# Kernel tuning notes

Hardware: AMD Instinct MI355X
Metric: run time of the kernel (lower is better)

The kernel has to match this reference:

```python
import jax, jax.numpy as jnp
import numpy as np

B, N, EMB, H, DH = 1, 196, 256, 8, 32
HID = 4 * EMB
EPS = 1e-5
SCALE = 16.0  # emb_size ** 0.5 (torch code scales by emb_size, not head_dim)


def _ln(x, w, b):
    m = jnp.mean(x, axis=-1, keepdims=True)
    v = jnp.mean((x - m) ** 2, axis=-1, keepdims=True)
    return (x - m) * jax.lax.rsqrt(v + EPS) * w + b


def _qkv(x, W, bias):
    # rearrange 'b n (h d qkv) -> qkv b h n d'
    t = (x @ W + bias).reshape(B, N, H, DH, 3)
    t = jnp.transpose(t, (4, 0, 2, 1, 3))
    return t[0], t[1], t[2]


def _attn(q, k, v, Wp, bp):
    att = jax.nn.softmax(jnp.einsum('bhqd,bhkd->bhqk', q, k) / SCALE, axis=-1)
    o = jnp.einsum('bhqk,bhkd->bhqd', att, v)
    o = jnp.transpose(o, (0, 2, 1, 3)).reshape(B, N, EMB)  # b n (h d)
    return o @ Wp + bp


def _ff(x, W1, b1, W2, b2):
    return jax.nn.gelu(x @ W1 + b1, approximate=False) @ W2 + b2


def _recon(x):
    x = x.reshape(B, 14, 14, 16, 16)
    x = jnp.transpose(x, (0, 3, 4, 1, 2))
    return x.reshape(B, 1, 224, 224)


def setup_inputs() -> dict:
    key = jax.random.key(0)
    ks = jax.random.split(key, 16)
    rn = lambda k, shape: jax.random.normal(k, shape, jnp.float32) * 0.02
    d = {
        'vis_emb': jax.random.normal(ks[0], (B, N, EMB), jnp.float32),
        'ir_emb': jax.random.normal(ks[1], (B, N, EMB), jnp.float32),
        'ln1v_w': jnp.ones((EMB,), jnp.float32), 'ln1v_b': jnp.zeros((EMB,), jnp.float32),
        'ln1i_w': jnp.ones((EMB,), jnp.float32), 'ln1i_b': jnp.zeros((EMB,), jnp.float32),
        'ln2v_w': jnp.ones((EMB,), jnp.float32), 'ln2v_b': jnp.zeros((EMB,), jnp.float32),
        'ln2i_w': jnp.ones((EMB,), jnp.float32), 'ln2i_b': jnp.zeros((EMB,), jnp.float32),
        'Wqkv_v': rn(ks[2], (EMB, 3 * EMB)), 'bqkv_v': jnp.zeros((3 * EMB,), jnp.float32),
        'Wqkv_i': rn(ks[3], (EMB, 3 * EMB)), 'bqkv_i': jnp.zeros((3 * EMB,), jnp.float32),
        'Wp_v': rn(ks[4], (EMB, EMB)), 'bp_v': jnp.zeros((EMB,), jnp.float32),
        'Wp_i': rn(ks[5], (EMB, EMB)), 'bp_i': jnp.zeros((EMB,), jnp.float32),
        'W1v': rn(ks[6], (EMB, HID)), 'b1v': jnp.zeros((HID,), jnp.float32),
        'W2v': rn(ks[7], (HID, EMB)), 'b2v': jnp.zeros((EMB,), jnp.float32),
        'W1i': rn(ks[8], (EMB, HID)), 'b1i': jnp.zeros((HID,), jnp.float32),
        'W2i': rn(ks[9], (HID, EMB)), 'b2i': jnp.zeros((EMB,), jnp.float32),
    }
    return d


def reference(vis_emb, ir_emb, ln1v_w, ln1v_b, ln1i_w, ln1i_b, ln2v_w, ln2v_b,
              ln2i_w, ln2i_b, Wqkv_v, bqkv_v, Wqkv_i, bqkv_i, Wp_v, bp_v,
              Wp_i, bp_i, W1v, b1v, W2v, b2v, W1i, b1i, W2i, b2i):
    nv = _ln(vis_emb, ln1v_w, ln1v_b)
    ni = _ln(ir_emb, ln1i_w, ln1i_b)
    qv, kv_, vv = _qkv(vis_emb, Wqkv_v, bqkv_v)
    qi, ki, vi = _qkv(ir_emb, Wqkv_i, bqkv_i)
    cross_v2i = _attn(qv, ki, vi, Wp_v, bp_v)   # vis queries attend ir k/v
    cross_i2v = _attn(qi, kv_, vv, Wp_i, bp_i)  # ir queries attend vis k/v
    rv = nv + cross_v2i
    ri = ni + cross_i2v
    lv = _ln(rv, ln2v_w, ln2v_b)
    li = _ln(ri, ln2i_w, ln2i_b)
    ov = _ff(lv, W1v, b1v, W2v, b2v) + lv
    oi = _ff(li, W1i, b1i, W2i, b2i) + li
    return jnp.concatenate([_recon(oi), _recon(ov)], axis=1)  # (1,2,224,224)
```

## Files before the change

### kernel.cpp

```cpp
#include <hip/hip_runtime.h>
#include <math.h>

#define NT   196
#define EMB  256
#define NH   8
#define DH   32
#define HID  1024
#define EPSV 1e-5f

#define GEMM_PANEL(Wptr, ldw, xsT, pp, cq, ks, KITER)                          \
    {                                                                          \
        const float* Wb = (Wptr);                                              \
        float4 a0 = {0,0,0,0}, a1 = a0, a2 = a0, a3 = a0;                      \
        _Pragma("unroll 8")                                                    \
        for (int kk = (ks) * (KITER); kk < (ks) * (KITER) + (KITER); kk++) {   \
            float4 w4 = *(const float4*)&Wb[kk * (ldw)];                       \
            float4 xr = *(const float4*)&(xsT)[kk * 4];                        \
            a0.x = fmaf(xr.x, w4.x, a0.x); a0.y = fmaf(xr.x, w4.y, a0.y);      \
            a0.z = fmaf(xr.x, w4.z, a0.z); a0.w = fmaf(xr.x, w4.w, a0.w);      \
            a1.x = fmaf(xr.y, w4.x, a1.x); a1.y = fmaf(xr.y, w4.y, a1.y);      \
            a1.z = fmaf(xr.y, w4.z, a1.z); a1.w = fmaf(xr.y, w4.w, a1.w);      \
            a2.x = fmaf(xr.z, w4.x, a2.x); a2.y = fmaf(xr.z, w4.y, a2.y);      \
            a2.z = fmaf(xr.z, w4.z, a2.z); a2.w = fmaf(xr.z, w4.w, a2.w);      \
            a3.x = fmaf(xr.w, w4.x, a3.x); a3.y = fmaf(xr.w, w4.y, a3.y);      \
            a3.z = fmaf(xr.w, w4.z, a3.z); a3.w = fmaf(xr.w, w4.w, a3.w);      \
        }                                                                      \
        *(float4*)&(pp)[((ks) * 4 + 0) * 256 + (cq) * 4] = a0;                 \
        *(float4*)&(pp)[((ks) * 4 + 1) * 256 + (cq) * 4] = a1;                 \
        *(float4*)&(pp)[((ks) * 4 + 2) * 256 + (cq) * 4] = a2;                 \
        *(float4*)&(pp)[((ks) * 4 + 3) * 256 + (cq) * 4] = a3;                 \
    }

__global__ __launch_bounds__(256) void k1_qkv(
    const float* __restrict__ vis, const float* __restrict__ ir,
    const float* __restrict__ Wqkv_v, const float* __restrict__ bqkv_v,
    const float* __restrict__ Wqkv_i, const float* __restrict__ bqkv_i,
    float* __restrict__ Q, float* __restrict__ Kq, float* __restrict__ Vq)
{
    const int b = blockIdx.x;
    const int s = b / 147;
    const int rem = b % 147;
    const int n0 = (rem / 3) * 4;
    const int cg = rem % 3;
    const int t = threadIdx.x;

    const float* x    = (s == 0) ? vis    : ir;
    const float* W    = (s == 0) ? Wqkv_v : Wqkv_i;
    const float* bias = (s == 0) ? bqkv_v : bqkv_i;

    __shared__ float xsT[EMB * 4];
    __shared__ float pp[4 * 4 * 256];

    {
        int r = t >> 6, c4 = (t & 63) * 4;
        float4 xv = *(const float4*)&x[(n0 + r) * EMB + c4];
        xsT[(c4 + 0) * 4 + r] = xv.x;
        xsT[(c4 + 1) * 4 + r] = xv.y;
        xsT[(c4 + 2) * 4 + r] = xv.z;
        xsT[(c4 + 3) * 4 + r] = xv.w;
    }
    __syncthreads();

    const int cq = t & 63, ks = t >> 6;
    GEMM_PANEL(W + cg * 256 + cq * 4, 768, xsT, pp, cq, ks, 64);
    __syncthreads();

    const int col = cg * 256 + t;
    const int h = col / 96, rr = col % 96, d = rr / 3, q = rr % 3;
    float* dst = (q == 0) ? Q : (q == 1 ? Kq : Vq);
    const float bval = bias[col];
    #pragma unroll
    for (int r = 0; r < 4; r++) {
        float v = pp[(0 * 4 + r) * 256 + t] + pp[(1 * 4 + r) * 256 + t]
                + pp[(2 * 4 + r) * 256 + t] + pp[(3 * 4 + r) * 256 + t] + bval;
        dst[((s * NH + h) * NT + n0 + r) * DH + d] = v;
    }
}

__global__ __launch_bounds__(256) void k2_attn(
    const float* __restrict__ Q, const float* __restrict__ Kq,
    const float* __restrict__ Vq, float* __restrict__ AO)
{
    const int b  = blockIdx.x;
    const int s  = b / 112;
    const int rm = b % 112;
    const int h  = rm / 14;
    const int rt = rm % 14;
    const int t    = threadIdx.x;
    const int wv   = t >> 6;
    const int lane = t & 63;

    __shared__ float kl[NT * 33];
    __shared__ float vl[NT * 33];
    __shared__ float pb[4][NT];

    const float4* Ks4 = (const float4*)(Kq + ((1 - s) * NH + h) * NT * DH);
    const float4* Vs4 = (const float4*)(Vq + ((1 - s) * NH + h) * NT * DH);
    for (int idx = t; idx < NT * 8; idx += 256) {
        int j = idx >> 3, d4 = (idx & 7) * 4;
        float4 kv = Ks4[idx];
        kl[j * 33 + d4 + 0] = kv.x; kl[j * 33 + d4 + 1] = kv.y;
        kl[j * 33 + d4 + 2] = kv.z; kl[j * 33 + d4 + 3] = kv.w;
        float4 vv = Vs4[idx];
        vl[j * 33 + d4 + 0] = vv.x; vl[j * 33 + d4 + 1] = vv.y;
        vl[j * 33 + d4 + 2] = vv.z; vl[j * 33 + d4 + 3] = vv.w;
    }
    __syncthreads();

    const float* Qs = Q + ((s * NH + h) * NT) * DH;
    const bool v3 = (lane + 192) < NT;
    const int  j3 = v3 ? (lane + 192) : 0;

    for (int it = 0; it < 4; it++) {
        int lr = it * 4 + wv;
        bool act = lr < 14;
        int i = rt * 14 + lr;
        float inv_sum = 0.0f;
        if (act) {
            float qreg[DH];
            #pragma unroll
            for (int d = 0; d < DH; d++) qreg[d] = Qs[i * DH + d];
            float s0 = 0.f, s1 = 0.f, s2 = 0.f, s3 = 0.f;
            #pragma unroll
            for (int d = 0; d < DH; d++) {
                float qd = qreg[d];
                s0 = fmaf(qd, kl[(lane      ) * 33 + d], s0);
                s1 = fmaf(qd, kl[(lane +  64) * 33 + d], s1);
                s2 = fmaf(qd, kl[(lane + 128) * 33 + d], s2);
                s3 = fmaf(qd, kl[ j3          * 33 + d], s3);
            }
            const float sc = 1.0f / 16.0f;
            s0 *= sc; s1 *= sc; s2 *= sc; s3 *= sc;
            float m = fmaxf(fmaxf(s0, s1), v3 ? fmaxf(s2, s3) : s2);
            #pragma unroll
            for (int mk = 32; mk >= 1; mk >>= 1) m = fmaxf(m, __shfl_xor(m, mk));
            float p0 = expf(s0 - m), p1 = expf(s1 - m), p2 = expf(s2 - m);
            float p3 = v3 ? expf(s3 - m) : 0.0f;
            float ls = p0 + p1 + p2 + p3;
            #pragma unroll
            for (int mk = 32; mk >= 1; mk >>= 1) ls += __shfl_xor(ls, mk);
            inv_sum = 1.0f / ls;
            pb[wv][lane]       = p0;
            pb[wv][lane +  64] = p1;
            pb[wv][lane + 128] = p2;
            if (v3) pb[wv][lane + 192] = p3;
        }
        __syncthreads();
        if (act) {
            int d = lane & 31, half = lane >> 5;
            float o = 0.0f;
            int jb = half * 98;
            for (int jj = 0; jj < 98; jj++) {
                int j = jb + jj;
                o = fmaf(pb[wv][j], vl[j * 33 + d], o);
            }
            o += __shfl_xor(o, 32);
            if (lane < 32) AO[(s * NT + i) * EMB + h * DH + d] = o * inv_sum;
        }
        __syncthreads();
    }
}

__global__ __launch_bounds__(256) void k3_tail(
    const float* __restrict__ vis, const float* __restrict__ ir,
    const float* __restrict__ AO,
    const float* __restrict__ ln1v_w, const float* __restrict__ ln1v_b,
    const float* __restrict__ ln1i_w, const float* __restrict__ ln1i_b,
    const float* __restrict__ Wp_v, const float* __restrict__ bp_v,
    const float* __restrict__ Wp_i, const float* __restrict__ bp_i,
    const float* __restrict__ ln2v_w, const float* __restrict__ ln2v_b,
    const float* __restrict__ ln2i_w, const float* __restrict__ ln2i_b,
    const float* __restrict__ W1v, const float* __restrict__ b1v,
    const float* __restrict__ W1i, const float* __restrict__ b1i,
    const float* __restrict__ W2v, const float* __restrict__ b2v,
    const float* __restrict__ W2i, const float* __restrict__ b2i,
    float* __restrict__ out)
{
    const int b = blockIdx.x;
    const int s = b / 49;
    const int n0 = (b % 49) * 4;
    const int t = threadIdx.x;

    const float* x   = (s == 0) ? vis    : ir;
    const float* Wp  = (s == 0) ? Wp_v   : Wp_i;
    const float* bp  = (s == 0) ? bp_v   : bp_i;
    const float* l1w = (s == 0) ? ln1v_w : ln1i_w;
    const float* l1b = (s == 0) ? ln1v_b : ln1i_b;
    const float* l2w = (s == 0) ? ln2v_w : ln2i_w;
    const float* l2b = (s == 0) ? ln2v_b : ln2i_b;
    const float* W1  = (s == 0) ? W1v    : W1i;
    const float* bb1 = (s == 0) ? b1v    : b1i;
    const float* W2  = (s == 0) ? W2v    : W2i;
    const float* bb2 = (s == 0) ? b2v    : b2i;

    __shared__ float smem[13312];
    float* aoT  = smem;
    float* nvb  = smem + 1024;
    float* rbuf = smem + 2048;
    float* lvb  = smem + 3072;
    float* lvT  = smem + 4096;
    float* hhT  = smem + 5120;
    float* pp   = smem + 9216;

    const int r = t >> 6, lane = t & 63, c4 = lane * 4;
    const int cq = t & 63, ks = t >> 6;

    {
        float4 xv = *(const float4*)&x[(n0 + r) * EMB + c4];
        float sum = xv.x + xv.y + xv.z + xv.w;
        float sq  = xv.x*xv.x + xv.y*xv.y + xv.z*xv.z + xv.w*xv.w;
        #pragma unroll
        for (int mk = 32; mk >= 1; mk >>= 1) {
            sum += __shfl_xor(sum, mk);
            sq  += __shfl_xor(sq,  mk);
        }
        float mean = sum * (1.0f / EMB);
        float inv  = rsqrtf(sq * (1.0f / EMB) - mean * mean + EPSV);
        float4 wv4 = *(const float4*)&l1w[c4];
        float4 bv4 = *(const float4*)&l1b[c4];
        nvb[r * 256 + c4 + 0] = (xv.x - mean) * inv * wv4.x + bv4.x;
        nvb[r * 256 + c4 + 1] = (xv.y - mean) * inv * wv4.y + bv4.y;
        nvb[r * 256 + c4 + 2] = (xv.z - mean) * inv * wv4.z + bv4.z;
        nvb[r * 256 + c4 + 3] = (xv.w - mean) * inv * wv4.w + bv4.w;
        float4 av = *(const float4*)&AO[(s * NT + n0 + r) * EMB + c4];
        aoT[(c4 + 0) * 4 + r] = av.x;
        aoT[(c4 + 1) * 4 + r] = av.y;
        aoT[(c4 + 2) * 4 + r] = av.z;
        aoT[(c4 + 3) * 4 + r] = av.w;
    }
    __syncthreads();

    GEMM_PANEL(Wp + cq * 4, EMB, aoT, pp, cq, ks, 64);
    __syncthreads();

    {
        const float bval = bp[t];
        #pragma unroll
        for (int r2 = 0; r2 < 4; r2++) {
            float v = pp[(0 * 4 + r2) * 256 + t] + pp[(1 * 4 + r2) * 256 + t]
                    + pp[(2 * 4 + r2) * 256 + t] + pp[(3 * 4 + r2) * 256 + t]
                    + bval + nvb[r2 * 256 + t];
            rbuf[r2 * 256 + t] = v;
        }
    }
    __syncthreads();
    {
        float4 rv = *(const float4*)&rbuf[r * 256 + c4];
        float sum = rv.x + rv.y + rv.z + rv.w;
        float sq  = rv.x*rv.x + rv.y*rv.y + rv.z*rv.z + rv.w*rv.w;
        #pragma unroll
        for (int mk = 32; mk >= 1; mk >>= 1) {
            sum += __shfl_xor(sum, mk);
            sq  += __shfl_xor(sq,  mk);
        }
        float mean = sum * (1.0f / EMB);
        float inv  = rsqrtf(sq * (1.0f / EMB) - mean * mean + EPSV);
        float4 wv4 = *(const float4*)&l2w[c4];
        float4 bv4 = *(const float4*)&l2b[c4];
        float4 o;
        o.x = (rv.x - mean) * inv * wv4.x + bv4.x;
        o.y = (rv.y - mean) * inv * wv4.y + bv4.y;
        o.z = (rv.z - mean) * inv * wv4.z + bv4.z;
        o.w = (rv.w - mean) * inv * wv4.w + bv4.w;
        *(float4*)&lvb[r * 256 + c4] = o;
        lvT[(c4 + 0) * 4 + r] = o.x;
        lvT[(c4 + 1) * 4 + r] = o.y;
        lvT[(c4 + 2) * 4 + r] = o.z;
        lvT[(c4 + 3) * 4 + r] = o.w;
    }
    __syncthreads();

    {
        const int cD = t * 4;
        float4 a0 = {0,0,0,0}, a1 = a0, a2 = a0, a3 = a0;
        #pragma unroll 8
        for (int kk = 0; kk < EMB; kk++) {
            float4 w4 = *(const float4*)&W1[kk * HID + cD];
            float4 xr = *(const float4*)&lvT[kk * 4];
            a0.x = fmaf(xr.x, w4.x, a0.x); a0.y = fmaf(xr.x, w4.y, a0.y);
            a0.z = fmaf(xr.x, w4.z, a0.z); a0.w = fmaf(xr.x, w4.w, a0.w);
            a1.x = fmaf(xr.y, w4.x, a1.x); a1.y = fmaf(xr.y, w4.y, a1.y);
            a1.z = fmaf(xr.y, w4.z, a1.z); a1.w = fmaf(xr.y, w4.w, a1.w);
            a2.x = fmaf(xr.z, w4.x, a2.x); a2.y = fmaf(xr.z, w4.y, a2.y);
            a2.z = fmaf(xr.z, w4.z, a2.z); a2.w = fmaf(xr.z, w4.w, a2.w);
            a3.x = fmaf(xr.w, w4.x, a3.x); a3.y = fmaf(xr.w, w4.y, a3.y);
            a3.z = fmaf(xr.w, w4.z, a3.z); a3.w = fmaf(xr.w, w4.w, a3.w);
        }
        float4 bv4 = *(const float4*)&bb1[cD];
        a0.x += bv4.x; a0.y += bv4.y; a0.z += bv4.z; a0.w += bv4.w;
        a1.x += bv4.x; a1.y += bv4.y; a1.z += bv4.z; a1.w += bv4.w;
        a2.x += bv4.x; a2.y += bv4.y; a2.z += bv4.z; a2.w += bv4.w;
        a3.x += bv4.x; a3.y += bv4.y; a3.z += bv4.z; a3.w += bv4.w;
        const float k = 0.7071067811865475f;
        #define GELU(v) (0.5f * (v) * (1.0f + erff((v) * k)))
        float4 h0 = { GELU(a0.x), GELU(a1.x), GELU(a2.x), GELU(a3.x) };
        float4 h1 = { GELU(a0.y), GELU(a1.y), GELU(a2.y), GELU(a3.y) };
        float4 h2 = { GELU(a0.z), GELU(a1.z), GELU(a2.z), GELU(a3.z) };
        float4 h3 = { GELU(a0.w), GELU(a1.w), GELU(a2.w), GELU(a3.w) };
        #undef GELU
        *(float4*)&hhT[(cD + 0) * 4] = h0;
        *(float4*)&hhT[(cD + 1) * 4] = h1;
        *(float4*)&hhT[(cD + 2) * 4] = h2;
        *(float4*)&hhT[(cD + 3) * 4] = h3;
    }
    __syncthreads();

    GEMM_PANEL(W2 + cq * 4, EMB, hhT, pp, cq, ks, 256);
    __syncthreads();
    {
        const float bval = bb2[t];
        const int p1 = t >> 4, p2 = t & 15;
        const int ch = (s == 0) ? 1 : 0;
        #pragma unroll
        for (int r2 = 0; r2 < 4; r2++) {
            int n = n0 + r2;
            float v = pp[(0 * 4 + r2) * 256 + t] + pp[(1 * 4 + r2) * 256 + t]
                    + pp[(2 * 4 + r2) * 256 + t] + pp[(3 * 4 + r2) * 256 + t]
                    + bval + lvb[r2 * 256 + t];
            int n1 = n / 14, n2 = n % 14;
            int f = p1 * 3136 + p2 * 196 + n1 * 14 + n2;
            out[ch * 50176 + f] = v;
        }
    }
}

extern "C" void kernel_launch(void* const* d_in, const int* in_sizes, int n_in,
                              void* d_out, int out_size, void* d_ws, size_t ws_size,
                              hipStream_t stream)
{
    const float* vis    = (const float*)d_in[0];
    const float* ir     = (const float*)d_in[1];
    const float* ln1v_w = (const float*)d_in[2];
    const float* ln1v_b = (const float*)d_in[3];
    const float* ln1i_w = (const float*)d_in[4];
    const float* ln1i_b = (const float*)d_in[5];
    const float* ln2v_w = (const float*)d_in[6];
    const float* ln2v_b = (const float*)d_in[7];
    const float* ln2i_w = (const float*)d_in[8];
    const float* ln2i_b = (const float*)d_in[9];
    const float* Wqkv_v = (const float*)d_in[10];
    const float* bqkv_v = (const float*)d_in[11];
    const float* Wqkv_i = (const float*)d_in[12];
    const float* bqkv_i = (const float*)d_in[13];
    const float* Wp_v   = (const float*)d_in[14];
    const float* bp_v   = (const float*)d_in[15];
    const float* Wp_i   = (const float*)d_in[16];
    const float* bp_i   = (const float*)d_in[17];
    const float* W1v    = (const float*)d_in[18];
    const float* b1v    = (const float*)d_in[19];
    const float* W2v    = (const float*)d_in[20];
    const float* b2v    = (const float*)d_in[21];
    const float* W1i    = (const float*)d_in[22];
    const float* b1i    = (const float*)d_in[23];
    const float* W2i    = (const float*)d_in[24];
    const float* b2i    = (const float*)d_in[25];

    float* ws = (float*)d_ws;
    float* Q  = ws;
    float* K  = ws + 100352;
    float* V  = ws + 200704;
    float* AO = ws + 301056;

    k1_qkv<<<294, 256, 0, stream>>>(vis, ir, Wqkv_v, bqkv_v, Wqkv_i, bqkv_i, Q, K, V);
    k2_attn<<<224, 256, 0, stream>>>(Q, K, V, AO);
    k3_tail<<<98, 256, 0, stream>>>(vis, ir, AO,
                                    ln1v_w, ln1v_b, ln1i_w, ln1i_b,
                                    Wp_v, bp_v, Wp_i, bp_i,
                                    ln2v_w, ln2v_b, ln2i_w, ln2i_b,
                                    W1v, b1v, W1i, b1i,
                                    W2v, b2v, W2i, b2i,
                                    (float*)d_out);
}
```

Baseline: 162.0 us.

## Split FFN into separate kernel parallelized over hidden chunks with atomic accumulation

The fused tail kernel is split in two. The first kernel runs the projection and both layernorms, writes the normalized rows to workspace, and initializes the output with residual plus bias. A new FFN kernel launches 392 blocks, one per 4 rows and one of four 256-wide hidden chunks, and accumulates the partial second-GEMM results into the output with atomicAdd. This raises parallelism from 98 blocks, but adds a launch, a workspace round trip, atomics, and a summation order that is no longer deterministic.

```diff
diff --git a/kernel.cpp b/kernel.cpp
--- a/kernel.cpp
+++ b/kernel.cpp
@@ -161,7 +161,7 @@
     }
 }
 
-__global__ __launch_bounds__(256) void k3_tail(
+__global__ __launch_bounds__(256) void k3_projln(
     const float* __restrict__ vis, const float* __restrict__ ir,
     const float* __restrict__ AO,
     const float* __restrict__ ln1v_w, const float* __restrict__ ln1v_b,
@@ -170,11 +170,8 @@
     const float* __restrict__ Wp_i, const float* __restrict__ bp_i,
     const float* __restrict__ ln2v_w, const float* __restrict__ ln2v_b,
     const float* __restrict__ ln2i_w, const float* __restrict__ ln2i_b,
-    const float* __restrict__ W1v, const float* __restrict__ b1v,
-    const float* __restrict__ W1i, const float* __restrict__ b1i,
-    const float* __restrict__ W2v, const float* __restrict__ b2v,
-    const float* __restrict__ W2i, const float* __restrict__ b2i,
-    float* __restrict__ out)
+    const float* __restrict__ b2v, const float* __restrict__ b2i,
+    float* __restrict__ LV, float* __restrict__ out)
 {
     const int b = blockIdx.x;
     const int s = b / 49;
@@ -188,19 +185,12 @@
     const float* l1b = (s == 0) ? ln1v_b : ln1i_b;
     const float* l2w = (s == 0) ? ln2v_w : ln2i_w;
     const float* l2b = (s == 0) ? ln2v_b : ln2i_b;
-    const float* W1  = (s == 0) ? W1v    : W1i;
-    const float* bb1 = (s == 0) ? b1v    : b1i;
-    const float* W2  = (s == 0) ? W2v    : W2i;
     const float* bb2 = (s == 0) ? b2v    : b2i;
 
-    __shared__ float smem[13312];
-    float* aoT  = smem;
-    float* nvb  = smem + 1024;
-    float* rbuf = smem + 2048;
-    float* lvb  = smem + 3072;
-    float* lvT  = smem + 4096;
-    float* hhT  = smem + 5120;
-    float* pp   = smem + 9216;
+    __shared__ float aoT[EMB * 4];
+    __shared__ float nvb[4 * 256];
+    __shared__ float rbuf[4 * 256];
+    __shared__ float pp[4 * 4 * 256];
 
     const int r = t >> 6, lane = t & 63, c4 = lane * 4;
     const int cq = t & 63, ks = t >> 6;
@@ -262,64 +252,86 @@
         o.y = (rv.y - mean) * inv * wv4.y + bv4.y;
         o.z = (rv.z - mean) * inv * wv4.z + bv4.z;
         o.w = (rv.w - mean) * inv * wv4.w + bv4.w;
-        *(float4*)&lvb[r * 256 + c4] = o;
-        lvT[(c4 + 0) * 4 + r] = o.x;
-        lvT[(c4 + 1) * 4 + r] = o.y;
-        lvT[(c4 + 2) * 4 + r] = o.z;
-        lvT[(c4 + 3) * 4 + r] = o.w;
-    }
-    __syncthreads();
-
-    {
-        const int cD = t * 4;
-        float4 a0 = {0,0,0,0}, a1 = a0, a2 = a0, a3 = a0;
-        #pragma unroll 8
-        for (int kk = 0; kk < EMB; kk++) {
-            float4 w4 = *(const float4*)&W1[kk * HID + cD];
-            float4 xr = *(const float4*)&lvT[kk * 4];
-            a0.x = fmaf(xr.x, w4.x, a0.x); a0.y = fmaf(xr.x, w4.y, a0.y);
-            a0.z = fmaf(xr.x, w4.z, a0.z); a0.w = fmaf(xr.x, w4.w, a0.w);
-            a1.x = fmaf(xr.y, w4.x, a1.x); a1.y = fmaf(xr.y, w4.y, a1.y);
-            a1.z = fmaf(xr.y, w4.z, a1.z); a1.w = fmaf(xr.y, w4.w, a1.w);
-            a2.x = fmaf(xr.z, w4.x, a2.x); a2.y = fmaf(xr.z, w4.y, a2.y);
-            a2.z = fmaf(xr.z, w4.z, a2.z); a2.w = fmaf(xr.z, w4.w, a2.w);
-            a3.x = fmaf(xr.w, w4.x, a3.x); a3.y = fmaf(xr.w, w4.y, a3.y);
-            a3.z = fmaf(xr.w, w4.z, a3.z); a3.w = fmaf(xr.w, w4.w, a3.w);
-        }
-        float4 bv4 = *(const float4*)&bb1[cD];
-        a0.x += bv4.x; a0.y += bv4.y; a0.z += bv4.z; a0.w += bv4.w;
-        a1.x += bv4.x; a1.y += bv4.y; a1.z += bv4.z; a1.w += bv4.w;
-        a2.x += bv4.x; a2.y += bv4.y; a2.z += bv4.z; a2.w += bv4.w;
-        a3.x += bv4.x; a3.y += bv4.y; a3.z += bv4.z; a3.w += bv4.w;
-        const float k = 0.7071067811865475f;
-        #define GELU(v) (0.5f * (v) * (1.0f + erff((v) * k)))
-        float4 h0 = { GELU(a0.x), GELU(a1.x), GELU(a2.x), GELU(a3.x) };
-        float4 h1 = { GELU(a0.y), GELU(a1.y), GELU(a2.y), GELU(a3.y) };
-        float4 h2 = { GELU(a0.z), GELU(a1.z), GELU(a2.z), GELU(a3.z) };
-        float4 h3 = { GELU(a0.w), GELU(a1.w), GELU(a2.w), GELU(a3.w) };
-        #undef GELU
-        *(float4*)&hhT[(cD + 0) * 4] = h0;
-        *(float4*)&hhT[(cD + 1) * 4] = h1;
-        *(float4*)&hhT[(cD + 2) * 4] = h2;
-        *(float4*)&hhT[(cD + 3) * 4] = h3;
-    }
-    __syncthreads();
-
-    GEMM_PANEL(W2 + cq * 4, EMB, hhT, pp, cq, ks, 256);
-    __syncthreads();
-    {
-        const float bval = bb2[t];
+        *(float4*)&LV[(s * NT + n0 + r) * EMB + c4] = o;
+        const int n = n0 + r;
+        const int n1 = n / 14, n2 = n % 14;
+        const int ch = (s == 0) ? 1 : 0;
+        float4 b4 = *(const float4*)&bb2[c4];
+        float bv[4] = { o.x + b4.x, o.y + b4.y, o.z + b4.z, o.w + b4.w };
+        #pragma unroll
+        for (int j = 0; j < 4; j++) {
+            int col = c4 + j;
+            int p1 = col >> 4, p2 = col & 15;
+            out[ch * 50176 + p1 * 3136 + p2 * 196 + n1 * 14 + n2] = bv[j];
+        }
+    }
+}
+
+__global__ __launch_bounds__(256) void k4_ffn(
+    const float* __restrict__ LV,
+    const float* __restrict__ W1v, const float* __restrict__ b1v,
+    const float* __restrict__ W1i, const float* __restrict__ b1i,
+    const float* __restrict__ W2v, const float* __restrict__ W2i,
+    float* __restrict__ out)
+{
+    const int b = blockIdx.x;
+    const int s = b / 196;
+    const int rem = b % 196;
+    const int n0 = (rem / 4) * 4;
+    const int col0 = (rem % 4) * 256;
+    const int t = threadIdx.x;
+
+    const float* W1  = (s == 0) ? W1v : W1i;
+    const float* bb1 = (s == 0) ? b1v : b1i;
+    const float* W2  = (s == 0) ? W2v : W2i;
+
+    __shared__ float lvT[EMB * 4];
+    __shared__ float hhT[256 * 4];
+    __shared__ float pp[4 * 4 * 256];
+
+    {
+        int r = t >> 6, c4 = (t & 63) * 4;
+        float4 xv = *(const float4*)&LV[(s * NT + n0 + r) * EMB + c4];
+        lvT[(c4 + 0) * 4 + r] = xv.x;
+        lvT[(c4 + 1) * 4 + r] = xv.y;
+        lvT[(c4 + 2) * 4 + r] = xv.z;
+        lvT[(c4 + 3) * 4 + r] = xv.w;
+    }
+    __syncthreads();
+
+    const int cq = t & 63, ks = t >> 6;
+
+    GEMM_PANEL(W1 + col0 + cq * 4, HID, lvT, pp, cq, ks, 64);
+    __syncthreads();
+
+    {
+        const float bval = bb1[col0 + t];
+        const float kg = 0.7071067811865475f;
+        float4 h;
+        #pragma unroll
+        for (int r = 0; r < 4; r++) {
+            float v = pp[(0 * 4 + r) * 256 + t] + pp[(1 * 4 + r) * 256 + t]
+                    + pp[(2 * 4 + r) * 256 + t] + pp[(3 * 4 + r) * 256 + t] + bval;
+            ((float*)&h)[r] = 0.5f * v * (1.0f + erff(v * kg));
+        }
+        *(float4*)&hhT[t * 4] = h;
+    }
+    __syncthreads();
+
+    GEMM_PANEL(W2 + col0 * EMB + cq * 4, EMB, hhT, pp, cq, ks, 64);
+    __syncthreads();
+
+    {
         const int p1 = t >> 4, p2 = t & 15;
         const int ch = (s == 0) ? 1 : 0;
         #pragma unroll
-        for (int r2 = 0; r2 < 4; r2++) {
-            int n = n0 + r2;
-            float v = pp[(0 * 4 + r2) * 256 + t] + pp[(1 * 4 + r2) * 256 + t]
-                    + pp[(2 * 4 + r2) * 256 + t] + pp[(3 * 4 + r2) * 256 + t]
-                    + bval + lvb[r2 * 256 + t];
+        for (int r = 0; r < 4; r++) {
+            int n = n0 + r;
+            float v = pp[(0 * 4 + r) * 256 + t] + pp[(1 * 4 + r) * 256 + t]
+                    + pp[(2 * 4 + r) * 256 + t] + pp[(3 * 4 + r) * 256 + t];
             int n1 = n / 14, n2 = n % 14;
             int f = p1 * 3136 + p2 * 196 + n1 * 14 + n2;
-            out[ch * 50176 + f] = v;
+            atomicAdd(&out[ch * 50176 + f], v);
         }
     }
 }
@@ -360,14 +372,15 @@
     float* K  = ws + 100352;
     float* V  = ws + 200704;
     float* AO = ws + 301056;
+    float* LV = ws + 401408;
 
     k1_qkv<<<294, 256, 0, stream>>>(vis, ir, Wqkv_v, bqkv_v, Wqkv_i, bqkv_i, Q, K, V);
     k2_attn<<<224, 256, 0, stream>>>(Q, K, V, AO);
-    k3_tail<<<98, 256, 0, stream>>>(vis, ir, AO,
-                                    ln1v_w, ln1v_b, ln1i_w, ln1i_b,
-                                    Wp_v, bp_v, Wp_i, bp_i,
-                                    ln2v_w, ln2v_b, ln2i_w, ln2i_b,
-                                    W1v, b1v, W1i, b1i,
-                                    W2v, b2v, W2i, b2i,
+    k3_projln<<<98, 256, 0, stream>>>(vis, ir, AO,
+                                      ln1v_w, ln1v_b, ln1i_w, ln1i_b,
+                                      Wp_v, bp_v, Wp_i, bp_i,
+                                      ln2v_w, ln2v_b, ln2i_w, ln2i_b,
+                                      b2v, b2i, LV, (float*)d_out);
+    k4_ffn<<<392, 256, 0, stream>>>(LV, W1v, b1v, W1i, b1i, W2v, W2i,
                                     (float*)d_out);
 }
```

Result: slower. 182.4 us (+12.5%).
